# Kernel optimization log

Hardware: AMD Instinct MI355X
Metric: run time of the kernel (lower is better)

Reference implementation:

```python
import jax, jax.numpy as jnp
import numpy as np

N, E, F_IN, D, K, OUT = 50000, 800000, 16, 64, 3, 3


def _safe_dinv(deg):
    safe = jnp.where(deg > 0, deg, 1.0)
    return jnp.where(deg > 0, jax.lax.rsqrt(safe), 0.0)


def _gcn(x, src, dst, W, b, n):
    # GCNConv(improved=True): A_hat = A + 2I, sym normalization
    xw = x @ W
    ones = jnp.ones(src.shape[0], x.dtype)
    deg = jax.ops.segment_sum(ones, dst, num_segments=n) + 2.0  # self-loop weight 2
    dinv = jax.lax.rsqrt(deg)  # deg >= 2, always finite
    agg = jax.ops.segment_sum((dinv[src] * dinv[dst])[:, None] * xw[src], dst, num_segments=n)
    agg = agg + (2.0 * dinv * dinv)[:, None] * xw  # self-loop contribution
    return agg + b


def _cheb(x, src, dst, dinv, W, b, n):
    # ChebConv, normalization='sym', lambda_max=2.0  =>  L_hat = -D^{-1/2} A D^{-1/2}
    coef = (dinv[src] * dinv[dst])[:, None]

    def lhat(z):
        return -jax.ops.segment_sum(coef * z[src], dst, num_segments=n)

    z_prev = x
    out = x @ W[0]
    z_cur = lhat(x)
    out = out + z_cur @ W[1]
    for k in range(2, W.shape[0]):
        z_next = 2.0 * lhat(z_cur) - z_prev
        out = out + z_next @ W[k]
        z_prev, z_cur = z_cur, z_next
    return out + b


def _gclstm(x, H, C, src, dst, dinv, wx, bx, wh, bh, wc, bg, n):
    # gate order in stacks: [i, f, c, o]; peephole wc: [i, f, o]
    gx = lambda g: _cheb(x, src, dst, dinv, wx[g], bx[g], n)
    gh = lambda g: _cheb(H, src, dst, dinv, wh[g], bh[g], n)
    i = jax.nn.sigmoid(gx(0) + gh(0) + wc[0] * C + bg[0])
    f = jax.nn.sigmoid(gx(1) + gh(1) + wc[1] * C + bg[1])
    t = jnp.tanh(gx(2) + gh(2) + bg[2])
    Cn = f * C + i * t
    o = jax.nn.sigmoid(gx(3) + gh(3) + wc[2] * Cn + bg[3])
    return o * jnp.tanh(Cn), Cn


def _forward(x, edge_index, p):
    (w_gcn1, b_gcn1, w_gcn2, b_gcn2,
     wx1, bx1, wh1, bh1, wc1, bg1,
     wx2, bx2, wh2, bh2, wc2, bg2,
     wx3, bx3, wh3, bh3, wc3, bg3,
     lin_w, lin_b) = p
    src, dst = edge_index[0], edge_index[1]
    n = x.shape[0]
    ones = jnp.ones(src.shape[0], x.dtype)
    deg_c = jax.ops.segment_sum(ones, dst, num_segments=n)  # Cheb: no self loops
    dinv_c = _safe_dinv(deg_c)

    h = jax.nn.relu(_gcn(x, src, dst, w_gcn1, b_gcn1, n))
    h = jax.nn.relu(_gcn(h, src, dst, w_gcn2, b_gcn2, n))

    z = jnp.zeros((n, wh1.shape[-1]), h.dtype)  # H=C=None -> zeros per cell
    H1, _ = _gclstm(h, z, z, src, dst, dinv_c, wx1, bx1, wh1, bh1, wc1, bg1, n)
    H2, _ = _gclstm(H1, z, z, src, dst, dinv_c, wx2, bx2, wh2, bh2, wc2, bg2, n)
    H3, _ = _gclstm(H2, z, z, src, dst, dinv_c, wx3, bx3, wh3, bh3, wc3, bg3, n)
    return jax.nn.relu(H3) @ lin_w + lin_b


def setup_inputs() -> dict:
    key = jax.random.key(0)

    def nrm(i, shape):
        return 0.1 * jax.random.normal(jax.random.fold_in(key, i), shape, jnp.float32)

    inp = {}
    inp["x"] = jax.random.normal(jax.random.fold_in(key, 0), (N, F_IN), jnp.float32)
    inp["edge_index"] = jax.random.randint(jax.random.fold_in(key, 1), (2, E), 0, N)
    inp["w_gcn1"] = nrm(2, (F_IN, D))
    inp["b_gcn1"] = nrm(3, (D,))
    inp["w_gcn2"] = nrm(4, (D, D))
    inp["b_gcn2"] = nrm(5, (D,))
    i = 6
    for l in (1, 2, 3):
        inp[f"wx{l}"] = nrm(i, (4, K, D, D)); i += 1
        inp[f"bx{l}"] = nrm(i, (4, D)); i += 1
        inp[f"wh{l}"] = nrm(i, (4, K, D, D)); i += 1
        inp[f"bh{l}"] = nrm(i, (4, D)); i += 1
        inp[f"wc{l}"] = nrm(i, (3, D)); i += 1
        inp[f"bg{l}"] = nrm(i, (4, D)); i += 1
    inp["lin_w"] = nrm(i, (D, OUT))
    inp["lin_b"] = nrm(i + 1, (OUT,))
    return inp


def reference(x, edge_index, w_gcn1, b_gcn1, w_gcn2, b_gcn2,
              wx1, bx1, wh1, bh1, wc1, bg1,
              wx2, bx2, wh2, bh2, wc2, bg2,
              wx3, bx3, wh3, bh3, wc3, bg3,
              lin_w, lin_b):
    p = (w_gcn1, b_gcn1, w_gcn2, b_gcn2,
         wx1, bx1, wh1, bh1, wc1, bg1,
         wx2, bx2, wh2, bh2, wc2, bg2,
         wx3, bx3, wh3, bh3, wc3, bg3,
         lin_w, lin_b)
    return _forward(x, edge_index, p)
```

## Files before the change

### kernel.cpp

```cpp
#include <hip/hip_runtime.h>


typedef _Float16 half8 __attribute__((ext_vector_type(8)));
typedef float f32x4 __attribute__((ext_vector_type(4)));

__global__ void count_deg_x_kernel(const int* __restrict__ ei, int* __restrict__ deg,
                                   int E, int chunk) {
  int range = blockIdx.x & 7;
  int lo = range * chunk, hi = lo + chunk;
  int stride = (gridDim.x >> 3) * blockDim.x;
  for (int e = (blockIdx.x >> 3) * blockDim.x + threadIdx.x; e < E; e += stride) {
    int d = ei[E + e];
    if (d >= lo && d < hi) atomicAdd(&deg[d], 1);
  }
}

__global__ void fill_x_kernel(const int* __restrict__ ei, int* __restrict__ cursor,
                              unsigned short* __restrict__ csr, int E, int chunk) {
  int range = blockIdx.x & 7;
  int lo = range * chunk, hi = lo + chunk;
  int stride = (gridDim.x >> 3) * blockDim.x;
  for (int e = (blockIdx.x >> 3) * blockDim.x + threadIdx.x; e < E; e += stride) {
    int d = ei[E + e];
    if (d >= lo && d < hi) {
      int pos = atomicAdd(&cursor[d], 1);
      csr[pos] = (unsigned short)ei[e];
    }
  }
}

__global__ void prep_kernel(const float* __restrict__ wx0, const float* __restrict__ wx1,
                            const float* __restrict__ wx2, const float* __restrict__ Wg2,
                            _Float16* __restrict__ Wpk, _Float16* __restrict__ Wpk2,
                            int* __restrict__ deg, int n) {
  int idx = blockIdx.x * 256 + threadIdx.x;
  if (idx < 110592) {
    int l = idx / 36864;
    int r = idx % 36864;
    int g = r / 12288;
    int r2 = r % 12288;
    int k = r2 / 64;
    int nn = r2 % 64;
    const float* wx = (l == 0) ? wx0 : (l == 1 ? wx1 : wx2);
    int gs = (g == 0) ? 0 : (g == 1 ? 2 : 3);
    int tau = k >> 6, kd = k & 63;
    size_t base = ((size_t)gs * 3) * 4096 + (size_t)kd * 64 + nn;
    float v;
    if (tau == 0)      v = wx[base] - wx[base + 2 * 4096];
    else if (tau == 1) v = wx[base + 1 * 4096];
    else               v = 2.f * wx[base + 2 * 4096];
    int kc = k >> 5, klo = k & 31;
    int lane = ((klo >> 3) << 4) | (nn & 15);
    int j = klo & 7;
    int nt = nn >> 4;
    Wpk[((((size_t)l * 3 + g) * 6 + kc) * 4 + nt) * 512 + (size_t)lane * 8 + j] = (_Float16)v;
  } else if (idx < 114688) {
    int i2 = idx - 110592;
    int k = i2 >> 6, nn = i2 & 63;
    float v = Wg2[k * 64 + nn];
    int kc = k >> 5, klo = k & 31;
    int lane = ((klo >> 3) << 4) | (nn & 15);
    int j = klo & 7;
    int nt = nn >> 4;
    Wpk2[(((size_t)kc * 4 + nt) * 64 + lane) * 8 + j] = (_Float16)v;
  } else if (idx < 114688 + n) {
    deg[idx - 114688] = 0;
  }
}

__global__ void sums_cast_kernel(const int* __restrict__ deg, int* __restrict__ bsum, int nsb,
                                 const float* __restrict__ x, _Float16* __restrict__ x16s,
                                 int n) {
  int tid = threadIdx.x;
  if ((int)blockIdx.x < nsb) {
    int i = blockIdx.x * 256 + tid;
    int v = (i < n) ? deg[i] : 0;
    for (int off = 32; off; off >>= 1) v += __shfl_down(v, off);
    __shared__ int ws[4];
    int lane = tid & 63, wid = tid >> 6;
    if (lane == 0) ws[wid] = v;
    __syncthreads();
    if (tid == 0) bsum[blockIdx.x] = ws[0] + ws[1] + ws[2] + ws[3];
  } else {
    int i = (blockIdx.x - nsb) * 256 + tid;
    if (i < n * 16) x16s[i] = (_Float16)(rsqrtf((float)deg[i >> 4] + 2.f) * x[i]);
  }
}

__global__ void scan_final(const int* __restrict__ deg, const int* __restrict__ bsum, int nb,
                           int* __restrict__ rowptr, int* __restrict__ cursor,
                           float* __restrict__ dg, float* __restrict__ dc,
                           float* __restrict__ rc, int n) {
  __shared__ int tmp[256];
  __shared__ int ws[4];
  __shared__ int base_sh;
  int tid = threadIdx.x;
  int v0 = (tid < nb && tid < (int)blockIdx.x) ? bsum[tid] : 0;
  for (int off = 32; off; off >>= 1) v0 += __shfl_down(v0, off);
  if ((tid & 63) == 0) ws[tid >> 6] = v0;
  __syncthreads();
  if (tid == 0) base_sh = ws[0] + ws[1] + ws[2] + ws[3];
  int i = blockIdx.x * 256 + tid;
  int v = (i < n) ? deg[i] : 0;
  tmp[tid] = v;
  __syncthreads();
  for (int off = 1; off < 256; off <<= 1) {
    int t = (tid >= off) ? tmp[tid - off] : 0;
    __syncthreads();
    tmp[tid] += t;
    __syncthreads();
  }
  if (i < n) {
    int excl = tmp[tid] - v + base_sh;
    rowptr[i] = excl;
    cursor[i] = excl;
    dg[i] = rsqrtf((float)v + 2.f);
    dc[i] = (v > 0) ? rsqrtf((float)v) : 0.f;
    rc[i] = (v > 0) ? sqrtf((float)v) : 0.f;
  }
}

__global__ __launch_bounds__(256) void gcn1_fused_kernel(
    const _Float16* __restrict__ X16s, const float* __restrict__ W1,
    const float* __restrict__ b1, const float* __restrict__ dg,
    _Float16* __restrict__ OUTs,
    const int* __restrict__ rowptr, const int* __restrict__ deg,
    const unsigned short* __restrict__ csr, int n) {
  __shared__ float w1s[16 * 64];
  int tid = threadIdx.x;
  for (int i = tid; i < 1024; i += 256) w1s[i] = W1[i];
  __syncthreads();
  int node = blockIdx.x * 8 + (tid >> 5);
  if (node >= n) return;
  int lane = tid & 63;
  int l32 = tid & 31;
  int eg = l32 >> 1, c8 = l32 & 1;
  int beg = rowptr[node], dgg = deg[node];
  const half8* IN8 = (const half8*)X16s;
  int idx = 0;
  if (l32 < dgg) idx = csr[beg + l32];
  float acc[8];
#pragma unroll
  for (int j = 0; j < 8; ++j) acc[j] = 0.f;
  int kmaxU = (dgg + 15) >> 4; if (kmaxU > 2) kmaxU = 2;
  for (int k = 0; k < kmaxU; ++k) {
    int s = __shfl(idx, eg + 16 * k, 32);
    half8 v = IN8[(size_t)s * 2 + c8];
    if (eg + 16 * k < dgg) {
#pragma unroll
      for (int j = 0; j < 8; ++j) acc[j] += (float)v[j];
    }
  }
  for (int p = beg + eg + 32; p < beg + dgg; p += 16) {
    int s = csr[p];
    half8 v = IN8[(size_t)s * 2 + c8];
#pragma unroll
    for (int j = 0; j < 8; ++j) acc[j] += (float)v[j];
  }
#pragma unroll
  for (int j = 0; j < 8; ++j) {
    acc[j] += __shfl_xor(acc[j], 2);
    acc[j] += __shfl_xor(acc[j], 4);
    acc[j] += __shfl_xor(acc[j], 8);
    acc[j] += __shfl_xor(acc[j], 16);
  }
  float dt = dg[node];
  half8 self = IN8[(size_t)node * 2 + c8];
  float v8[8];
#pragma unroll
  for (int j = 0; j < 8; ++j) v8[j] = dt * acc[j] + 2.f * dt * (float)self[j];
  float agg[16];
  int base = lane & 32;
#pragma unroll
  for (int k = 0; k < 16; ++k) agg[k] = __shfl(v8[k & 7], base + (k >> 3));
  float h0 = b1[l32], h1 = b1[l32 + 32];
#pragma unroll
  for (int k = 0; k < 16; ++k) {
    h0 += agg[k] * w1s[k * 64 + l32];
    h1 += agg[k] * w1s[k * 64 + l32 + 32];
  }
  OUTs[(size_t)node * 64 + l32]      = (_Float16)(dt * fmaxf(h0, 0.f));
  OUTs[(size_t)node * 64 + l32 + 32] = (_Float16)(dt * fmaxf(h1, 0.f));
}

template <int MODE>
__global__ void gather_kernel(const int* __restrict__ rowptr, const int* __restrict__ deg,
                              const unsigned short* __restrict__ csr,
                              const float* __restrict__ dinv,
                              const _Float16* __restrict__ INs,
                              _Float16* __restrict__ OUT, int n) {
  int node = blockIdx.x * (blockDim.x >> 6) + (threadIdx.x >> 6);
  if (node >= n) return;
  int lane = threadIdx.x & 63;
  int eg = lane >> 3, c8 = lane & 7;
  int beg = rowptr[node], dgg = deg[node];
  const half8* IN8 = (const half8*)INs;
  int idx = 0;
  if (lane < dgg) idx = csr[beg + lane];
  float acc[8], acc2[8];
#pragma unroll
  for (int j = 0; j < 8; ++j) { acc[j] = 0.f; acc2[j] = 0.f; }
  int kmaxU = (dgg + 7) >> 3; if (kmaxU > 8) kmaxU = 8;
  int k = 0;
  for (; k + 2 <= kmaxU; k += 2) {
    int s0 = __shfl(idx, eg + 8 * k);
    int s1 = __shfl(idx, eg + 8 * k + 8);
    half8 v0 = IN8[(size_t)s0 * 8 + c8];
    half8 v1 = IN8[(size_t)s1 * 8 + c8];
    if (eg + 8 * k < dgg) {
#pragma unroll
      for (int j = 0; j < 8; ++j) acc[j] += (float)v0[j];
    }
    if (eg + 8 * k + 8 < dgg) {
#pragma unroll
      for (int j = 0; j < 8; ++j) acc2[j] += (float)v1[j];
    }
  }
  if (k < kmaxU) {
    int s = __shfl(idx, eg + 8 * k);
    half8 v = IN8[(size_t)s * 8 + c8];
    if (eg + 8 * k < dgg) {
#pragma unroll
      for (int j = 0; j < 8; ++j) acc[j] += (float)v[j];
    }
  }
  for (int p = beg + eg + 64; p < beg + dgg; p += 8) {
    int s = csr[p];
    half8 v = IN8[(size_t)s * 8 + c8];
#pragma unroll
    for (int j = 0; j < 8; ++j) acc[j] += (float)v[j];
  }
#pragma unroll
  for (int j = 0; j < 8; ++j) {
    acc[j] += acc2[j];
    acc[j] += __shfl_xor(acc[j], 8);
    acc[j] += __shfl_xor(acc[j], 16);
    acc[j] += __shfl_xor(acc[j], 32);
  }
  if (eg == 0) {
    float dt = dinv[node];
    size_t o8 = (size_t)node * 8 + c8;
    half8 r;
    if (MODE == 0) {
      half8 self = IN8[o8];
#pragma unroll
      for (int j = 0; j < 8; ++j) r[j] = (_Float16)(dt * acc[j] + 2.f * dt * (float)self[j]);
    } else if (MODE == 1) {
      float s = -dt * dt;
#pragma unroll
      for (int j = 0; j < 8; ++j) r[j] = (_Float16)(s * acc[j]);
    } else {
#pragma unroll
      for (int j = 0; j < 8; ++j) r[j] = (_Float16)(-dt * acc[j]);
    }
    ((half8*)OUT)[o8] = r;
  }
}

__global__ __launch_bounds__(256) void gcn2_mfma_kernel(
    const _Float16* __restrict__ A, const _Float16* __restrict__ W2,
    const float* __restrict__ bias, const float* __restrict__ dc,
    _Float16* __restrict__ OUT, _Float16* __restrict__ OUTs, int n) {
  int tid = threadIdx.x;
  int wid = tid >> 6, lane = tid & 63;
  int n0 = blockIdx.x * 64;
  int row = n0 + wid * 16 + (lane & 15);
  int rowc = min(row, n - 1);
  int ksub = (lane >> 4) << 3;
  int dbase = lane & 15;
  const _Float16* Wlane = W2 + (size_t)lane * 8;
  f32x4 acc[4];
#pragma unroll
  for (int nt = 0; nt < 4; ++nt) {
    float b = bias[nt * 16 + dbase];
    acc[nt] = (f32x4){b, b, b, b};
  }
#pragma unroll
  for (int kc = 0; kc < 2; ++kc) {
    half8 a = *(const half8*)&A[(size_t)rowc * 64 + (kc << 5) + ksub];
#pragma unroll
    for (int nt = 0; nt < 4; ++nt) {
      half8 b = *(const half8*)(Wlane + (size_t)(kc * 4 + nt) * 512);
      acc[nt] = __builtin_amdgcn_mfma_f32_16x16x32_f16(a, b, acc[nt], 0, 0, 0);
    }
  }
  int mrow = n0 + wid * 16 + ((lane >> 4) << 2);
#pragma unroll
  for (int nt = 0; nt < 4; ++nt) {
    int d = nt * 16 + dbase;
#pragma unroll
    for (int r = 0; r < 4; ++r) {
      int node = mrow + r;
      if (node < n) {
        float h = fmaxf(acc[nt][r], 0.f);
        OUT[(size_t)node * 64 + d] = (_Float16)h;
        OUTs[(size_t)node * 64 + d] = (_Float16)(dc[node] * h);
      }
    }
  }
}

template <int FINAL>
__global__ __launch_bounds__(256) void gate_mfma_kernel(
    const _Float16* __restrict__ X, const _Float16* __restrict__ Z1s,
    const _Float16* __restrict__ Y,
    const _Float16* __restrict__ Wl,
    const float* __restrict__ bx, const float* __restrict__ bh, const float* __restrict__ bg,
    const float* __restrict__ wc, const float* __restrict__ dc,
    const float* __restrict__ rinv,
    _Float16* __restrict__ H, _Float16* __restrict__ Hs,
    const float* __restrict__ lw, const float* __restrict__ lb,
    float* __restrict__ out, int n) {
  int tid = threadIdx.x;
  int wid = tid >> 6, lane = tid & 63;
  int n0 = blockIdx.x * 64;
  int row = n0 + wid * 16 + (lane & 15);
  int rowc = min(row, n - 1);
  int ksub = (lane >> 4) << 3;
  const _Float16* Wlane = Wl + (size_t)lane * 8;
  int dbase = lane & 15;
  float rv = rinv[rowc];

  f32x4 acc[3][4];
#pragma unroll
  for (int g = 0; g < 3; ++g) {
    int gs = (g == 0) ? 0 : (g == 1 ? 2 : 3);
#pragma unroll
    for (int nt = 0; nt < 4; ++nt) {
      int d = nt * 16 + dbase;
      float b = bx[gs * 64 + d] + bh[gs * 64 + d] + bg[gs * 64 + d];
      acc[g][nt] = (f32x4){b, b, b, b};
    }
  }
  const _Float16* T[3] = {X, Z1s, Y};
#pragma unroll
  for (int kc = 0; kc < 6; ++kc) {
    const _Float16* t = T[kc >> 1];
    half8 a = *(const half8*)&t[(size_t)rowc * 64 + ((kc & 1) << 5) + ksub];
    if (kc >= 2 && kc < 4) {
#pragma unroll
      for (int j = 0; j < 8; ++j) a[j] = (_Float16)((float)a[j] * rv);
    }
#pragma unroll
    for (int g = 0; g < 3; ++g) {
#pragma unroll
      for (int nt = 0; nt < 4; ++nt) {
        half8 b = *(const half8*)(Wlane + (size_t)((g * 6 + kc) * 4 + nt) * 512);
        acc[g][nt] = __builtin_amdgcn_mfma_f32_16x16x32_f16(a, b, acc[g][nt], 0, 0, 0);
      }
    }
  }
  int mrow = n0 + wid * 16 + ((lane >> 4) << 2);
  float po[4][3];
  if (FINAL) {
#pragma unroll
    for (int r = 0; r < 4; ++r) { po[r][0] = 0.f; po[r][1] = 0.f; po[r][2] = 0.f; }
  }
#pragma unroll
  for (int nt = 0; nt < 4; ++nt) {
    int d = nt * 16 + dbase;
    float wcd = wc[128 + d];
#pragma unroll
    for (int r = 0; r < 4; ++r) {
      float ig = 1.f / (1.f + expf(-acc[0][nt][r]));
      float tt = tanhf(acc[1][nt][r]);
      float Cn = ig * tt;
      float og = 1.f / (1.f + expf(-(acc[2][nt][r] + wcd * Cn)));
      float h = og * tanhf(Cn);
      if (FINAL) {
        float rl = fmaxf(h, 0.f);
        po[r][0] += rl * lw[d * 3 + 0];
        po[r][1] += rl * lw[d * 3 + 1];
        po[r][2] += rl * lw[d * 3 + 2];
      } else {
        int node = mrow + r;
        if (node < n) {
          H[(size_t)node * 64 + d] = (_Float16)h;
          Hs[(size_t)node * 64 + d] = (_Float16)(dc[node] * h);
        }
      }
    }
  }
  if (FINAL) {
#pragma unroll
    for (int m = 1; m < 16; m <<= 1) {
#pragma unroll
      for (int r = 0; r < 4; ++r) {
        po[r][0] += __shfl_xor(po[r][0], m);
        po[r][1] += __shfl_xor(po[r][1], m);
        po[r][2] += __shfl_xor(po[r][2], m);
      }
    }
    if (dbase == 0) {
#pragma unroll
      for (int r = 0; r < 4; ++r) {
        int node = mrow + r;
        if (node < n) {
          out[(size_t)node * 3 + 0] = po[r][0] + lb[0];
          out[(size_t)node * 3 + 1] = po[r][1] + lb[1];
          out[(size_t)node * 3 + 2] = po[r][2] + lb[2];
        }
      }
    }
  }
}

extern "C" void kernel_launch(void* const* d_in, const int* in_sizes, int n_in,
                              void* d_out, int out_size, void* d_ws, size_t ws_size,
                              hipStream_t stream) {
  const float* x      = (const float*)d_in[0];
  const int*   ei     = (const int*)d_in[1];
  const float* w_gcn1 = (const float*)d_in[2];
  const float* b_gcn1 = (const float*)d_in[3];
  const float* w_gcn2 = (const float*)d_in[4];
  const float* b_gcn2 = (const float*)d_in[5];
  const float* wx[3]  = {(const float*)d_in[6],  (const float*)d_in[12], (const float*)d_in[18]};
  const float* bx[3]  = {(const float*)d_in[7],  (const float*)d_in[13], (const float*)d_in[19]};
  const float* bh[3]  = {(const float*)d_in[9],  (const float*)d_in[15], (const float*)d_in[21]};
  const float* wc[3]  = {(const float*)d_in[10], (const float*)d_in[16], (const float*)d_in[22]};
  const float* bg[3]  = {(const float*)d_in[11], (const float*)d_in[17], (const float*)d_in[23]};
  const float* lin_w  = (const float*)d_in[24];
  const float* lin_b  = (const float*)d_in[25];
  float* out = (float*)d_out;

  int N = in_sizes[0] / 16;
  int E = in_sizes[1] / 2;
  int nsb = (N + 255) / 256;
  int chunk = (N + 7) / 8;

  char* ws = (char*)d_ws;
  size_t off = 0;
  auto alloc = [&](size_t bytes) {
    void* p = ws + off;
    off = (off + bytes + 255) & ~(size_t)255;
    return p;
  };
  int* deg        = (int*)alloc((size_t)N * 4);
  int* rowptr     = (int*)alloc((size_t)N * 4);
  int* cursor     = (int*)alloc((size_t)N * 4);
  int* bsum       = (int*)alloc((size_t)nsb * 4);
  unsigned short* csr = (unsigned short*)alloc((size_t)E * 2);
  float* dinv_g   = (float*)alloc((size_t)N * 4);
  float* dinv_c   = (float*)alloc((size_t)N * 4);
  float* rinv_c   = (float*)alloc((size_t)N * 4);
  _Float16* Wpk   = (_Float16*)alloc((size_t)3 * 36864 * 2);
  _Float16* Wpk2  = (_Float16*)alloc((size_t)4096 * 2);
  _Float16* x16s  = (_Float16*)alloc((size_t)N * 16 * 2);
  _Float16* bufA  = (_Float16*)alloc((size_t)N * 64 * 2);
  _Float16* bufAs = (_Float16*)alloc((size_t)N * 64 * 2);
  _Float16* bufB  = (_Float16*)alloc((size_t)N * 64 * 2);
  _Float16* bufC  = (_Float16*)alloc((size_t)N * 64 * 2);
  (void)ws_size; (void)n_in; (void)out_size;

  prep_kernel<<<(114688 + N + 255) / 256, 256, 0, stream>>>(wx[0], wx[1], wx[2], w_gcn2,
                                                            Wpk, Wpk2, deg, N);
  count_deg_x_kernel<<<4096, 256, 0, stream>>>(ei, deg, E, chunk);
  sums_cast_kernel<<<nsb + (N * 16 + 255) / 256, 256, 0, stream>>>(deg, bsum, nsb, x, x16s, N);
  scan_final<<<nsb, 256, 0, stream>>>(deg, bsum, nsb, rowptr, cursor,
                                      dinv_g, dinv_c, rinv_c, N);
  fill_x_kernel<<<4096, 256, 0, stream>>>(ei, cursor, csr, E, chunk);

  int nb64 = (N + 63) / 64;
  int nbw  = (N + 3) / 4;
  int nb8  = (N + 7) / 8;

  gcn1_fused_kernel<<<nb8, 256, 0, stream>>>(x16s, w_gcn1, b_gcn1, dinv_g, bufB,
                                             rowptr, deg, csr, N);
  gather_kernel<0><<<nbw, 256, 0, stream>>>(rowptr, deg, csr, dinv_g, bufB, bufC, N);
  gcn2_mfma_kernel<<<nb64, 256, 0, stream>>>(bufC, Wpk2, b_gcn2, dinv_c, bufA, bufAs, N);

  for (int l = 0; l < 3; ++l) {
    gather_kernel<1><<<nbw, 256, 0, stream>>>(rowptr, deg, csr, dinv_c, bufAs, bufB, N);
    gather_kernel<3><<<nbw, 256, 0, stream>>>(rowptr, deg, csr, dinv_c, bufB, bufC, N);
    if (l < 2) {
      gate_mfma_kernel<0><<<nb64, 256, 0, stream>>>(bufA, bufB, bufC, Wpk + (size_t)l * 36864,
                                                    bx[l], bh[l], bg[l], wc[l], dinv_c, rinv_c,
                                                    bufA, bufAs, nullptr, nullptr, nullptr, N);
    } else {
      gate_mfma_kernel<1><<<nb64, 256, 0, stream>>>(bufA, bufB, bufC, Wpk + (size_t)l * 36864,
                                                    bx[l], bh[l], bg[l], wc[l], dinv_c, rinv_c,
                                                    nullptr, nullptr, lin_w, lin_b, out, N);
    }
  }
}
```

Baseline: 345.3 us.

## Compact edge indices to 16-bit and sort CSR neighbor lists per node

The prep kernel now narrows the int32 edge index arrays into 16-bit src/dst copies. The degree-count and CSR-fill passes read these instead of the int32 array, which cuts the bytes each pass scans. A new bitonic sort kernel orders each node's neighbor list (degree 2..64) within a wavefront so that the later gather kernels touch memory in ascending order and get better cache locality. In exchange it adds an extra conversion pass over all edges and an extra sort launch.

```diff
diff --git a/kernel.cpp b/kernel.cpp
--- a/kernel.cpp
+++ b/kernel.cpp
@@ -4,35 +4,13 @@
 typedef _Float16 half8 __attribute__((ext_vector_type(8)));
 typedef float f32x4 __attribute__((ext_vector_type(4)));
 
-__global__ void count_deg_x_kernel(const int* __restrict__ ei, int* __restrict__ deg,
-                                   int E, int chunk) {
-  int range = blockIdx.x & 7;
-  int lo = range * chunk, hi = lo + chunk;
-  int stride = (gridDim.x >> 3) * blockDim.x;
-  for (int e = (blockIdx.x >> 3) * blockDim.x + threadIdx.x; e < E; e += stride) {
-    int d = ei[E + e];
-    if (d >= lo && d < hi) atomicAdd(&deg[d], 1);
-  }
-}
-
-__global__ void fill_x_kernel(const int* __restrict__ ei, int* __restrict__ cursor,
-                              unsigned short* __restrict__ csr, int E, int chunk) {
-  int range = blockIdx.x & 7;
-  int lo = range * chunk, hi = lo + chunk;
-  int stride = (gridDim.x >> 3) * blockDim.x;
-  for (int e = (blockIdx.x >> 3) * blockDim.x + threadIdx.x; e < E; e += stride) {
-    int d = ei[E + e];
-    if (d >= lo && d < hi) {
-      int pos = atomicAdd(&cursor[d], 1);
-      csr[pos] = (unsigned short)ei[e];
-    }
-  }
-}
-
 __global__ void prep_kernel(const float* __restrict__ wx0, const float* __restrict__ wx1,
                             const float* __restrict__ wx2, const float* __restrict__ Wg2,
+                            const int* __restrict__ ei,
                             _Float16* __restrict__ Wpk, _Float16* __restrict__ Wpk2,
-                            int* __restrict__ deg, int n) {
+                            int* __restrict__ deg,
+                            unsigned short* __restrict__ dst16,
+                            unsigned short* __restrict__ src16, int n, int E) {
   int idx = blockIdx.x * 256 + threadIdx.x;
   if (idx < 110592) {
     int l = idx / 36864;
@@ -65,7 +43,62 @@
     Wpk2[(((size_t)kc * 4 + nt) * 64 + lane) * 8 + j] = (_Float16)v;
   } else if (idx < 114688 + n) {
     deg[idx - 114688] = 0;
-  }
+  } else if (idx < 114688 + n + E) {
+    int e = idx - 114688 - n;
+    dst16[e] = (unsigned short)ei[E + e];
+  } else if (idx < 114688 + n + 2 * E) {
+    int e = idx - 114688 - n - E;
+    src16[e] = (unsigned short)ei[e];
+  }
+}
+
+__global__ void count_deg_x_kernel(const unsigned short* __restrict__ dst16,
+                                   int* __restrict__ deg, int E, int chunk) {
+  int range = blockIdx.x & 7;
+  int lo = range * chunk, hi = lo + chunk;
+  int stride = (gridDim.x >> 3) * blockDim.x;
+  for (int e = (blockIdx.x >> 3) * blockDim.x + threadIdx.x; e < E; e += stride) {
+    int d = dst16[e];
+    if (d >= lo && d < hi) atomicAdd(&deg[d], 1);
+  }
+}
+
+__global__ void fill_x_kernel(const unsigned short* __restrict__ dst16,
+                              const unsigned short* __restrict__ src16,
+                              int* __restrict__ cursor,
+                              unsigned short* __restrict__ csr, int E, int chunk) {
+  int range = blockIdx.x & 7;
+  int lo = range * chunk, hi = lo + chunk;
+  int stride = (gridDim.x >> 3) * blockDim.x;
+  for (int e = (blockIdx.x >> 3) * blockDim.x + threadIdx.x; e < E; e += stride) {
+    int d = dst16[e];
+    if (d >= lo && d < hi) {
+      int pos = atomicAdd(&cursor[d], 1);
+      csr[pos] = src16[e];
+    }
+  }
+}
+
+__global__ void sort_csr_kernel(const int* __restrict__ rowptr, const int* __restrict__ deg,
+                                unsigned short* __restrict__ csr, int n) {
+  int node = blockIdx.x * (blockDim.x >> 6) + (threadIdx.x >> 6);
+  if (node >= n) return;
+  int lane = threadIdx.x & 63;
+  int beg = rowptr[node], dgg = deg[node];
+  if (dgg > 64 || dgg < 2) return;
+  int v = (lane < dgg) ? (int)csr[beg + lane] : 0x7FFFFFFF;
+#pragma unroll
+  for (int size = 2; size <= 64; size <<= 1) {
+    bool desc = (lane & size) != 0;
+#pragma unroll
+    for (int stride = size >> 1; stride > 0; stride >>= 1) {
+      int pv = __shfl_xor(v, stride);
+      bool upper = (lane & stride) != 0;
+      int mn = min(v, pv), mx = max(v, pv);
+      v = (upper != desc) ? mx : mn;
+    }
+  }
+  if (lane < dgg) csr[beg + lane] = (unsigned short)v;
 }
 
 __global__ void sums_cast_kernel(const int* __restrict__ deg, int* __restrict__ bsum, int nsb,
@@ -439,7 +472,9 @@
   int* rowptr     = (int*)alloc((size_t)N * 4);
   int* cursor     = (int*)alloc((size_t)N * 4);
   int* bsum       = (int*)alloc((size_t)nsb * 4);
-  unsigned short* csr = (unsigned short*)alloc((size_t)E * 2);
+  unsigned short* csr   = (unsigned short*)alloc((size_t)E * 2);
+  unsigned short* dst16 = (unsigned short*)alloc((size_t)E * 2);
+  unsigned short* src16 = (unsigned short*)alloc((size_t)E * 2);
   float* dinv_g   = (float*)alloc((size_t)N * 4);
   float* dinv_c   = (float*)alloc((size_t)N * 4);
   float* rinv_c   = (float*)alloc((size_t)N * 4);
@@ -452,17 +487,19 @@
   _Float16* bufC  = (_Float16*)alloc((size_t)N * 64 * 2);
   (void)ws_size; (void)n_in; (void)out_size;
 
-  prep_kernel<<<(114688 + N + 255) / 256, 256, 0, stream>>>(wx[0], wx[1], wx[2], w_gcn2,
-                                                            Wpk, Wpk2, deg, N);
-  count_deg_x_kernel<<<4096, 256, 0, stream>>>(ei, deg, E, chunk);
+  int nbw  = (N + 3) / 4;
+  int nb64 = (N + 63) / 64;
+  int nb8  = (N + 7) / 8;
+
+  int prep_total = 114688 + N + 2 * E;
+  prep_kernel<<<(prep_total + 255) / 256, 256, 0, stream>>>(wx[0], wx[1], wx[2], w_gcn2, ei,
+                                                            Wpk, Wpk2, deg, dst16, src16, N, E);
+  count_deg_x_kernel<<<4096, 256, 0, stream>>>(dst16, deg, E, chunk);
   sums_cast_kernel<<<nsb + (N * 16 + 255) / 256, 256, 0, stream>>>(deg, bsum, nsb, x, x16s, N);
   scan_final<<<nsb, 256, 0, stream>>>(deg, bsum, nsb, rowptr, cursor,
                                       dinv_g, dinv_c, rinv_c, N);
-  fill_x_kernel<<<4096, 256, 0, stream>>>(ei, cursor, csr, E, chunk);
-
-  int nb64 = (N + 63) / 64;
-  int nbw  = (N + 3) / 4;
-  int nb8  = (N + 7) / 8;
+  fill_x_kernel<<<4096, 256, 0, stream>>>(dst16, src16, cursor, csr, E, chunk);
+  sort_csr_kernel<<<nbw, 256, 0, stream>>>(rowptr, deg, csr, N);
 
   gcn1_fused_kernel<<<nb8, 256, 0, stream>>>(x16s, w_gcn1, b_gcn1, dinv_g, bufB,
                                              rowptr, deg, csr, N);
```

After: 360.2 us. 1.04x slower.
